# Kernel optimization log

Hardware: AMD Instinct MI355X
Metric: run time of the kernel (lower is better)

## Reference

```python
import jax, jax.numpy as jnp
import numpy as np

N = 32768      # total points (multiple of patch_size -> no padding needed)
C = 768        # channels
H = 8          # num heads
K = 256        # patch_size (window length)
HD = C // H    # head dim = 96, divisible by 6 (3 axes * rotary pairs)
FREQ = 100.0   # rope_freq


def rope3d(x, pos):
    """Point-position RoPE: head dim split into 3 axis chunks, each rotated
    by angles pos_axis * freq**(-i/half).  x: [N,H,HD], pos: [N,3] float."""
    d_axis = HD // 3            # 32
    half = d_axis // 2          # 16
    inv_freq = FREQ ** (-jnp.arange(half, dtype=x.dtype) / half)   # [half]
    ang = pos[:, :, None] * inv_freq[None, None, :]                # [N,3,half]
    cos = jnp.cos(ang)[:, None, :, :]                              # [N,1,3,half]
    sin = jnp.sin(ang)[:, None, :, :]
    xr = x.reshape(x.shape[0], x.shape[1], 3, d_axis)              # [N,H,3,d_axis]
    x1, x2 = xr[..., :half], xr[..., half:]
    out = jnp.concatenate([x1 * cos - x2 * sin, x1 * sin + x2 * cos], axis=-1)
    return out.reshape(x.shape)


def setup_inputs() -> dict:
    key = jax.random.key(0)
    ks = jax.random.split(key, 6)
    feat = jax.random.normal(ks[0], (N, C), dtype=jnp.float32)
    grid_coord = jax.random.randint(ks[1], (N, 3), 0, 1024, dtype=jnp.int32)
    order = jax.random.permutation(ks[2], N).astype(jnp.int32)     # serialized order
    inverse = jnp.argsort(order).astype(jnp.int32)                 # its inverse
    w_qkv = jax.random.normal(ks[3], (C, 3 * C), dtype=jnp.float32) * 0.02
    b_qkv = jnp.zeros((3 * C,), dtype=jnp.float32)
    w_proj = jax.random.normal(ks[4], (C, C), dtype=jnp.float32) * 0.02
    b_proj = jnp.zeros((C,), dtype=jnp.float32)
    return {"feat": feat, "grid_coord": grid_coord, "order": order,
            "inverse": inverse, "w_qkv": w_qkv, "b_qkv": b_qkv,
            "w_proj": w_proj, "b_proj": b_proj}


def reference(feat, grid_coord, order, inverse, w_qkv, b_qkv, w_proj, b_proj):
    scale = HD ** -0.5
    P = N // K  # number of windows
    qkv = (feat @ w_qkv + b_qkv)[order]                   # gather by serialized order
    pos = grid_coord[order].astype(feat.dtype)            # [N,3]
    q, k, v = jnp.split(qkv, 3, axis=-1)
    q = rope3d(q.reshape(N, H, HD), pos)
    k = rope3d(k.reshape(N, H, HD), pos)
    v = v.reshape(N, H, HD)
    # windowed (varlen with equal patch lengths) attention
    qw = q.reshape(P, K, H, HD)
    kw = k.reshape(P, K, H, HD)
    vw = v.reshape(P, K, H, HD)
    logits = jnp.einsum('pqhd,pkhd->phqk', qw, kw) * scale
    attn = jax.nn.softmax(logits, axis=-1)
    out = jnp.einsum('phqk,pkhd->pqhd', attn, vw).reshape(N, C)
    out = out[inverse]                                    # scatter back to input order
    return out @ w_proj + b_proj
```

## Files before the change

### kernel.cpp

```cpp
#include <hip/hip_runtime.h>
#include <hip/hip_bf16.h>
#include <stdint.h>

typedef __bf16 bf16_t;
typedef __bf16 bf16x8 __attribute__((ext_vector_type(8)));
typedef __bf16 bf16x4 __attribute__((ext_vector_type(4)));
typedef float f32x4 __attribute__((ext_vector_type(4)));

template <int V> struct ic { static constexpr int value = V; };

__device__ __forceinline__ void gload_lds16(const bf16_t* g, bf16_t* l) {
  __builtin_amdgcn_global_load_lds((const __attribute__((address_space(1))) void*)g,
                                   (__attribute__((address_space(3))) void*)l, 16, 0, 0);
}

__global__ __launch_bounds__(256) void transpose_cast_k(const float* __restrict__ W,
                                                        bf16_t* __restrict__ Bt,
                                                        int KDin, int MDin) {
  __shared__ float tile[64][65];
  const int bm = blockIdx.x, bk = blockIdx.y;
  const int c = threadIdx.x & 63, r0 = threadIdx.x >> 6;
#pragma unroll
  for (int rr = 0; rr < 16; ++rr) {
    int row = rr * 4 + r0;
    tile[row][c] = W[(size_t)(bk * 64 + row) * MDin + bm * 64 + c];
  }
  __syncthreads();
#pragma unroll
  for (int rr = 0; rr < 16; ++rr) {
    int mo = rr * 4 + r0;
    Bt[(size_t)(bm * 64 + mo) * KDin + bk * 64 + c] = (bf16_t)tile[c][mo];
  }
}

__global__ __launch_bounds__(256) void gather_cast_k(const float* __restrict__ feat,
                                                     const int* __restrict__ order,
                                                     const int* __restrict__ grid_coord,
                                                     bf16_t* __restrict__ featp,
                                                     float* __restrict__ posf) {
  const int id = blockIdx.x * 256 + threadIdx.x;
  const int j = id / 192;
  const int c = (id % 192) * 4;
  const int g = order[j];
  const float4 v = *(const float4*)(feat + (size_t)g * 768 + c);
  bf16x4 o;
  o[0] = (bf16_t)v.x; o[1] = (bf16_t)v.y; o[2] = (bf16_t)v.z; o[3] = (bf16_t)v.w;
  *(bf16x4*)(featp + (size_t)j * 768 + c) = o;
  if (c == 0) {
    posf[j * 3 + 0] = (float)grid_coord[g * 3 + 0];
    posf[j * 3 + 1] = (float)grid_coord[g * 3 + 1];
    posf[j * 3 + 2] = (float)grid_coord[g * 3 + 2];
  }
}

template <int MODE, int NBX>
__global__ __launch_bounds__(512, 2) void gemm256_k(const bf16_t* __restrict__ A,
                                                    const bf16_t* __restrict__ Bt,
                                                    const float* __restrict__ bias,
                                                    bf16_t* __restrict__ Cq,
                                                    bf16_t* __restrict__ Ck,
                                                    bf16_t* __restrict__ Cv,
                                                    float* __restrict__ Cf,
                                                    const int* __restrict__ order,
                                                    const float* __restrict__ posf) {
  extern __shared__ bf16_t sm[];
  bf16_t* ldsA = sm;
  bf16_t* ldsB = sm + 4 * 8192;

  const int tid = threadIdx.x;
  const int lane = tid & 63, wave = tid >> 6;
  const int wr = wave >> 2, wc = wave & 3;
  const int lq = lane & 15, lk = lane >> 4;

  const int bid = blockIdx.x;
  const int cpx = gridDim.x >> 3;
  const int rm = (bid & 7) * cpx + (bid >> 3);
  const int by = rm / NBX, bx = rm % NBX;

  const int o0 = tid, o1 = tid + 512;
  const int r0s = o0 >> 2, ls0 = (o0 & 3) ^ ((r0s >> 1) & 3);
  const int r1s = o1 >> 2, ls1 = (o1 & 3) ^ ((r1s >> 1) & 3);
  const bf16_t* pA0 = A + (size_t)(by * 256 + r0s) * 768 + ls0 * 8;
  const bf16_t* pA1 = A + (size_t)(by * 256 + r1s) * 768 + ls1 * 8;
  const bf16_t* pB0 = Bt + (size_t)(bx * 256 + r0s) * 768 + ls0 * 8;
  const bf16_t* pB1 = Bt + (size_t)(bx * 256 + r1s) * 768 + ls1 * 8;

  auto stageA = [&](int kt) {
    bf16_t* d = ldsA + ((kt & 3) << 13);
    gload_lds16(pA0 + kt * 32, d + o0 * 8);
    gload_lds16(pA1 + kt * 32, d + o1 * 8);
  };
  auto stageB = [&](int kt) {
    bf16_t* d = ldsB + ((kt & 3) << 13);
    gload_lds16(pB0 + kt * 32, d + o0 * 8);
    gload_lds16(pB1 + kt * 32, d + o1 * 8);
  };

  const int pslot = lk ^ ((lq >> 1) & 3);

  f32x4 acc[8][4] = {};

  stageA(0); stageB(0); stageA(1); stageB(1); stageA(2); stageB(2);
  asm volatile("s_waitcnt vmcnt(8)" ::: "memory");
  __builtin_amdgcn_s_barrier();
  __builtin_amdgcn_sched_barrier(0);

  auto group = [&](int t, auto VMC, auto STGC) {
    constexpr int VM = decltype(VMC)::value;
    constexpr bool STG = decltype(STGC)::value;
    const bf16_t* Ab = ldsA + ((t & 3) << 13);
    const bf16_t* Bb = ldsB + ((t & 3) << 13);
    bf16x8 af[4], bfr[4];
#pragma unroll
    for (int m = 0; m < 4; ++m)
      af[m] = *(const bf16x8*)(Ab + (wr * 128 + m * 16 + lq) * 32 + pslot * 8);
#pragma unroll
    for (int n = 0; n < 4; ++n)
      bfr[n] = *(const bf16x8*)(Bb + (wc * 64 + n * 16 + lq) * 32 + pslot * 8);
    if constexpr (STG) stageA(t + 3);
    __builtin_amdgcn_s_barrier();
    asm volatile("s_waitcnt lgkmcnt(0)" ::: "memory");
    __builtin_amdgcn_s_setprio(1);
#pragma unroll
    for (int n = 0; n < 4; ++n)
#pragma unroll
      for (int m = 0; m < 4; ++m)
        acc[m][n] = __builtin_amdgcn_mfma_f32_16x16x32_bf16(af[m], bfr[n], acc[m][n], 0, 0, 0);
    __builtin_amdgcn_s_setprio(0);
    __builtin_amdgcn_s_barrier();
#pragma unroll
    for (int m = 0; m < 4; ++m)
      af[m] = *(const bf16x8*)(Ab + (wr * 128 + 64 + m * 16 + lq) * 32 + pslot * 8);
    if constexpr (STG) stageB(t + 3);
    if constexpr (VM == 8) asm volatile("s_waitcnt vmcnt(8)" ::: "memory");
    else if constexpr (VM == 4) asm volatile("s_waitcnt vmcnt(4)" ::: "memory");
    else if constexpr (VM == 0) asm volatile("s_waitcnt vmcnt(0)" ::: "memory");
    __builtin_amdgcn_s_barrier();
    asm volatile("s_waitcnt lgkmcnt(0)" ::: "memory");
    __builtin_amdgcn_s_setprio(1);
#pragma unroll
    for (int n = 0; n < 4; ++n)
#pragma unroll
      for (int m = 0; m < 4; ++m)
        acc[4 + m][n] = __builtin_amdgcn_mfma_f32_16x16x32_bf16(af[m], bfr[n], acc[4 + m][n], 0, 0, 0);
    __builtin_amdgcn_s_setprio(0);
    __builtin_amdgcn_s_barrier();
    __builtin_amdgcn_sched_barrier(0);
  };

  for (int t = 0; t < 21; ++t) group(t, ic<8>{}, ic<1>{});
  group(21, ic<4>{}, ic<0>{});
  group(22, ic<0>{}, ic<0>{});
  group(23, ic<-1>{}, ic<0>{});

  const int colb = bx * 256 + wc * 64;
  float bcol[4];
#pragma unroll
  for (int n = 0; n < 4; ++n) bcol[n] = bias[colb + n * 16 + lq];

  if (MODE == 0) {
    const int sec = bx / 3;
    const int coll = colb - sec * 768;
    if (sec < 2) {
      bf16_t* base = sec == 0 ? Cq : Ck;
      const int a0 = (colb % 96) >> 5;
      const int a1 = ((colb + 32) % 96) >> 5;
      const float fr = exp2f(-0.41524101186f * (float)lq);
#pragma unroll
      for (int m = 0; m < 8; ++m) {
        const int rowb = by * 256 + wr * 128 + m * 16 + lk * 4;
#pragma unroll
        for (int r = 0; r < 4; ++r) {
          const int row = rowb + r;
          float s0, c0, s1, c1;
          __sincosf(posf[row * 3 + a0] * fr, &s0, &c0);
          __sincosf(posf[row * 3 + a1] * fr, &s1, &c1);
          const float x1 = acc[m][0][r] + bcol[0], x2 = acc[m][1][r] + bcol[1];
          const float y1 = acc[m][2][r] + bcol[2], y2 = acc[m][3][r] + bcol[3];
          acc[m][0][r] = x1 * c0 - x2 * s0;
          acc[m][1][r] = x1 * s0 + x2 * c0;
          acc[m][2][r] = y1 * c1 - y2 * s1;
          acc[m][3][r] = y1 * s1 + y2 * c1;
        }
#pragma unroll
        for (int n = 0; n < 4; ++n) {
          const int col = coll + n * 16 + lq;
#pragma unroll
          for (int r = 0; r < 4; ++r)
            base[(size_t)(rowb + r) * 768 + col] = (bf16_t)acc[m][n][r];
        }
      }
    } else {
#pragma unroll
      for (int m = 0; m < 8; ++m) {
        const int rowb = by * 256 + wr * 128 + m * 16 + lk * 4;
#pragma unroll
        for (int n = 0; n < 4; ++n) {
          const int col = coll + n * 16 + lq;
          bf16x4 o;
#pragma unroll
          for (int r = 0; r < 4; ++r) o[r] = (bf16_t)(acc[m][n][r] + bcol[n]);
          *(bf16x4*)(Cv + (size_t)col * 32768 + rowb) = o;
        }
      }
    }
  } else {
#pragma unroll
    for (int m = 0; m < 8; ++m) {
      const int rowb = by * 256 + wr * 128 + m * 16 + lk * 4;
      int ro[4];
#pragma unroll
      for (int r = 0; r < 4; ++r) ro[r] = order[rowb + r];
#pragma unroll
      for (int n = 0; n < 4; ++n) {
        const int col = colb + n * 16 + lq;
#pragma unroll
        for (int r = 0; r < 4; ++r)
          Cf[(size_t)ro[r] * 768 + col] = acc[m][n][r] + bcol[n];
      }
    }
  }
}

__global__ __launch_bounds__(256) void attn_k(bf16_t* QO,
                                              const bf16_t* __restrict__ Kb,
                                              const bf16_t* __restrict__ Vt) {
  __shared__ bf16_t KV[24576];
  __shared__ bf16_t Pb[4][2048];
  const int bid = blockIdx.x;
  const int chunk = bid & 3;
  const int ph = bid >> 2;
  const int h = ph & 7, p = ph >> 3;
  const int tid = threadIdx.x, lane = tid & 63, wave = tid >> 6;
  const int lq = lane & 15, lk = lane >> 4;
  const int tok0 = p * 256;
  const int qrow0 = chunk * 64 + wave * 16;
  const float scale = 0.10206207262f;

#pragma unroll
  for (int i = 0; i < 12; ++i) {
    const int fi = i * 4 + wave;
    const int nt = fi / 3, a = fi - nt * 3;
    const bf16_t* src = Kb + (size_t)(tok0 + nt * 16 + (lane & 15)) * 768 +
                        h * 96 + a * 32 + (lane >> 4) * 8;
    gload_lds16(src, KV + i * 2048 + tid * 8);
  }
  bf16x8 aq[3];
  {
    const bf16_t* qb = QO + (size_t)(tok0 + qrow0 + lq) * 768 + h * 96 + lk * 8;
#pragma unroll
    for (int kc = 0; kc < 3; ++kc) aq[kc] = *(const bf16x8*)(qb + kc * 32);
  }
  __syncthreads();

  f32x4 sacc[16];
#pragma unroll
  for (int nt = 0; nt < 16; ++nt) {
    f32x4 acc = {0.f, 0.f, 0.f, 0.f};
#pragma unroll
    for (int kc = 0; kc < 3; ++kc) {
      bf16x8 bk = *(const bf16x8*)(KV + (size_t)((nt * 3 + kc) * 64 + lane) * 8);
      acc = __builtin_amdgcn_mfma_f32_16x16x32_bf16(aq[kc], bk, acc, 0, 0, 0);
    }
    sacc[nt] = acc;
  }
  __syncthreads();

#pragma unroll
  for (int i = 0; i < 12; ++i) {
    const int fi = i * 4 + wave;
    const int d = (fi >> 3) * 16 + (lane & 15);
    const int tb = (fi & 7) * 32 + (lane >> 4) * 8;
    const bf16_t* src = Vt + (size_t)(h * 96 + d) * 32768 + tok0 + tb;
    gload_lds16(src, KV + i * 2048 + tid * 8);
  }

  float linv[4];
#pragma unroll
  for (int r = 0; r < 4; ++r) {
    float mx = -1e30f;
#pragma unroll
    for (int nt = 0; nt < 16; ++nt) mx = fmaxf(mx, sacc[nt][r]);
    mx = fmaxf(mx, __shfl_xor(mx, 1));
    mx = fmaxf(mx, __shfl_xor(mx, 2));
    mx = fmaxf(mx, __shfl_xor(mx, 4));
    mx = fmaxf(mx, __shfl_xor(mx, 8));
    mx *= scale;
    float l = 0.f;
#pragma unroll
    for (int nt = 0; nt < 16; ++nt) {
      float e = __expf(sacc[nt][r] * scale - mx);
      sacc[nt][r] = e;
      l += e;
    }
    l += __shfl_xor(l, 1);
    l += __shfl_xor(l, 2);
    l += __shfl_xor(l, 4);
    l += __shfl_xor(l, 8);
    linv[r] = 1.f / l;
  }
  __syncthreads();

  bf16_t* pw = &Pb[wave][0];
  f32x4 oacc[6] = {};
#pragma unroll
  for (int hf = 0; hf < 2; ++hf) {
#pragma unroll
    for (int ntl = 0; ntl < 8; ++ntl) {
      const int nt = hf * 8 + ntl;
      const int chk = ntl * 2 + (lq >> 3);
#pragma unroll
      for (int r = 0; r < 4; ++r) {
        const int row = lk * 4 + r;
        const int phys = chk ^ (row & 7);
        pw[row * 128 + phys * 8 + (lq & 7)] = (bf16_t)sacc[nt][r];
      }
    }
#pragma unroll
    for (int kcl = 0; kcl < 4; ++kcl) {
      const int physr = (kcl * 4 + lk) ^ (lq & 7);
      bf16x8 pf = *(const bf16x8*)(pw + lq * 128 + physr * 8);
      const int kc = hf * 4 + kcl;
#pragma unroll
      for (int dt = 0; dt < 6; ++dt) {
        bf16x8 vb = *(const bf16x8*)(KV + (size_t)((dt * 8 + kc) * 64 + lane) * 8);
        oacc[dt] = __builtin_amdgcn_mfma_f32_16x16x32_bf16(pf, vb, oacc[dt], 0, 0, 0);
      }
    }
  }

#pragma unroll
  for (int dt = 0; dt < 6; ++dt) {
#pragma unroll
    for (int r = 0; r < 4; ++r) {
      const int row = tok0 + qrow0 + lk * 4 + r;
      QO[(size_t)row * 768 + h * 96 + dt * 16 + lq] = (bf16_t)(oacc[dt][r] * linv[r]);
    }
  }
}

extern "C" void kernel_launch(void* const* d_in, const int* in_sizes, int n_in,
                              void* d_out, int out_size, void* d_ws, size_t ws_size,
                              hipStream_t stream) {
  const float* feat       = (const float*)d_in[0];
  const int*   grid_coord = (const int*)d_in[1];
  const int*   order      = (const int*)d_in[2];
  const float* w_qkv      = (const float*)d_in[4];
  const float* b_qkv      = (const float*)d_in[5];
  const float* w_proj     = (const float*)d_in[6];
  const float* b_proj     = (const float*)d_in[7];
  float* out = (float*)d_out;

  char* ws = (char*)d_ws;
  bf16_t* Bt1   = (bf16_t*)(ws);
  bf16_t* Bt2   = (bf16_t*)(ws + 3538944);
  bf16_t* featp = (bf16_t*)(ws + 4718592);
  bf16_t* Qb    = (bf16_t*)(ws + 55050240);
  bf16_t* Kb    = (bf16_t*)(ws + 105381888);
  bf16_t* Vt    = (bf16_t*)(ws + 155713536);
  float*  posf  = (float*)(ws + 206045184);

  static bool attr_set = false;
  if (!attr_set) {
    (void)hipFuncSetAttribute((const void*)gemm256_k<0, 9>,
                              hipFuncAttributeMaxDynamicSharedMemorySize, 131072);
    (void)hipFuncSetAttribute((const void*)gemm256_k<1, 3>,
                              hipFuncAttributeMaxDynamicSharedMemorySize, 131072);
    attr_set = true;
  }

  transpose_cast_k<<<dim3(36, 12), 256, 0, stream>>>(w_qkv, Bt1, 768, 2304);
  transpose_cast_k<<<dim3(12, 12), 256, 0, stream>>>(w_proj, Bt2, 768, 768);
  gather_cast_k<<<24576, 256, 0, stream>>>(feat, order, grid_coord, featp, posf);
  gemm256_k<0, 9><<<1152, 512, 131072, stream>>>(featp, Bt1, b_qkv, Qb, Kb, Vt,
                                                 nullptr, nullptr, posf);
  attn_k<<<4096, 256, 0, stream>>>(Qb, Kb, Vt);
  gemm256_k<1, 3><<<384, 512, 131072, stream>>>(Qb, Bt2, b_proj, nullptr, nullptr,
                                                nullptr, out, order, nullptr);
}
```

Baseline: 483.7 us.

## Process full window per attention block and overlap V load with QK

The attention kernel now assigns one (window, head) pair per 512-thread block. Each of the 8 waves handles two 16-row query tiles, replacing four 256-thread blocks that each reloaded the same K and V tiles. K and V are loaded into separate regions of a 128KB dynamic LDS buffer up front. Split vmcnt waits let the V transfer overlap the first QK^T and softmax pass. This removes redundant global traffic for K/V, but the large LDS footprint limits residency to one block per CU, and each wave's two row tiles run serially.

Measured after the change: 484.3 us. About the same (+0.1%).

```diff
diff --git a/kernel.cpp b/kernel.cpp
--- a/kernel.cpp
+++ b/kernel.cpp
@@ -222,119 +222,127 @@
   }
 }
 
-__global__ __launch_bounds__(256) void attn_k(bf16_t* QO,
+__global__ __launch_bounds__(512) void attn_k(bf16_t* QO,
                                               const bf16_t* __restrict__ Kb,
                                               const bf16_t* __restrict__ Vt) {
-  __shared__ bf16_t KV[24576];
-  __shared__ bf16_t Pb[4][2048];
+  extern __shared__ bf16_t alds[];
+  bf16_t* Kreg = alds;
+  bf16_t* Vreg = alds + 24576;
   const int bid = blockIdx.x;
-  const int chunk = bid & 3;
-  const int ph = bid >> 2;
-  const int h = ph & 7, p = ph >> 3;
+  const int h = bid & 7, p = bid >> 3;
   const int tid = threadIdx.x, lane = tid & 63, wave = tid >> 6;
   const int lq = lane & 15, lk = lane >> 4;
   const int tok0 = p * 256;
-  const int qrow0 = chunk * 64 + wave * 16;
   const float scale = 0.10206207262f;
-
-#pragma unroll
-  for (int i = 0; i < 12; ++i) {
-    const int fi = i * 4 + wave;
+  bf16_t* pw = alds + 49152 + wave * 2048;
+
+  bf16x8 aq[2][3];
+#pragma unroll
+  for (int rb = 0; rb < 2; ++rb) {
+    const bf16_t* qb = QO + (size_t)(tok0 + wave * 32 + rb * 16 + lq) * 768 + h * 96 + lk * 8;
+#pragma unroll
+    for (int kc = 0; kc < 3; ++kc) aq[rb][kc] = *(const bf16x8*)(qb + kc * 32);
+  }
+  __builtin_amdgcn_sched_barrier(0);
+
+#pragma unroll
+  for (int i = 0; i < 6; ++i) {
+    const int fi = i * 8 + wave;
     const int nt = fi / 3, a = fi - nt * 3;
     const bf16_t* src = Kb + (size_t)(tok0 + nt * 16 + (lane & 15)) * 768 +
                         h * 96 + a * 32 + (lane >> 4) * 8;
-    gload_lds16(src, KV + i * 2048 + tid * 8);
-  }
-  bf16x8 aq[3];
-  {
-    const bf16_t* qb = QO + (size_t)(tok0 + qrow0 + lq) * 768 + h * 96 + lk * 8;
-#pragma unroll
-    for (int kc = 0; kc < 3; ++kc) aq[kc] = *(const bf16x8*)(qb + kc * 32);
-  }
-  __syncthreads();
-
-  f32x4 sacc[16];
-#pragma unroll
-  for (int nt = 0; nt < 16; ++nt) {
-    f32x4 acc = {0.f, 0.f, 0.f, 0.f};
-#pragma unroll
-    for (int kc = 0; kc < 3; ++kc) {
-      bf16x8 bk = *(const bf16x8*)(KV + (size_t)((nt * 3 + kc) * 64 + lane) * 8);
-      acc = __builtin_amdgcn_mfma_f32_16x16x32_bf16(aq[kc], bk, acc, 0, 0, 0);
-    }
-    sacc[nt] = acc;
-  }
-  __syncthreads();
-
-#pragma unroll
-  for (int i = 0; i < 12; ++i) {
-    const int fi = i * 4 + wave;
+    gload_lds16(src, Kreg + i * 4096 + tid * 8);
+  }
+#pragma unroll
+  for (int i = 0; i < 6; ++i) {
+    const int fi = i * 8 + wave;
     const int d = (fi >> 3) * 16 + (lane & 15);
     const int tb = (fi & 7) * 32 + (lane >> 4) * 8;
     const bf16_t* src = Vt + (size_t)(h * 96 + d) * 32768 + tok0 + tb;
-    gload_lds16(src, KV + i * 2048 + tid * 8);
-  }
-
-  float linv[4];
-#pragma unroll
-  for (int r = 0; r < 4; ++r) {
-    float mx = -1e30f;
-#pragma unroll
-    for (int nt = 0; nt < 16; ++nt) mx = fmaxf(mx, sacc[nt][r]);
-    mx = fmaxf(mx, __shfl_xor(mx, 1));
-    mx = fmaxf(mx, __shfl_xor(mx, 2));
-    mx = fmaxf(mx, __shfl_xor(mx, 4));
-    mx = fmaxf(mx, __shfl_xor(mx, 8));
-    mx *= scale;
-    float l = 0.f;
+    gload_lds16(src, Vreg + i * 4096 + tid * 8);
+  }
+
+  asm volatile("s_waitcnt vmcnt(6)" ::: "memory");
+  __builtin_amdgcn_s_barrier();
+
+#pragma unroll
+  for (int rb = 0; rb < 2; ++rb) {
+    f32x4 sacc[16];
 #pragma unroll
     for (int nt = 0; nt < 16; ++nt) {
-      float e = __expf(sacc[nt][r] * scale - mx);
-      sacc[nt][r] = e;
-      l += e;
-    }
-    l += __shfl_xor(l, 1);
-    l += __shfl_xor(l, 2);
-    l += __shfl_xor(l, 4);
-    l += __shfl_xor(l, 8);
-    linv[r] = 1.f / l;
-  }
-  __syncthreads();
-
-  bf16_t* pw = &Pb[wave][0];
-  f32x4 oacc[6] = {};
-#pragma unroll
-  for (int hf = 0; hf < 2; ++hf) {
-#pragma unroll
-    for (int ntl = 0; ntl < 8; ++ntl) {
-      const int nt = hf * 8 + ntl;
-      const int chk = ntl * 2 + (lq >> 3);
+      f32x4 acc = {0.f, 0.f, 0.f, 0.f};
+#pragma unroll
+      for (int kc = 0; kc < 3; ++kc) {
+        bf16x8 bk = *(const bf16x8*)(Kreg + (size_t)((nt * 3 + kc) * 64 + lane) * 8);
+        acc = __builtin_amdgcn_mfma_f32_16x16x32_bf16(aq[rb][kc], bk, acc, 0, 0, 0);
+      }
+      sacc[nt] = acc;
+    }
+
+    float linv[4];
+#pragma unroll
+    for (int r = 0; r < 4; ++r) {
+      float mx = -1e30f;
+#pragma unroll
+      for (int nt = 0; nt < 16; ++nt) mx = fmaxf(mx, sacc[nt][r]);
+      mx = fmaxf(mx, __shfl_xor(mx, 1));
+      mx = fmaxf(mx, __shfl_xor(mx, 2));
+      mx = fmaxf(mx, __shfl_xor(mx, 4));
+      mx = fmaxf(mx, __shfl_xor(mx, 8));
+      mx *= scale;
+      float l = 0.f;
+#pragma unroll
+      for (int nt = 0; nt < 16; ++nt) {
+        float e = __expf(sacc[nt][r] * scale - mx);
+        sacc[nt][r] = e;
+        l += e;
+      }
+      l += __shfl_xor(l, 1);
+      l += __shfl_xor(l, 2);
+      l += __shfl_xor(l, 4);
+      l += __shfl_xor(l, 8);
+      linv[r] = 1.f / l;
+    }
+
+    if (rb == 0) {
+      asm volatile("s_waitcnt vmcnt(0)" ::: "memory");
+      __builtin_amdgcn_s_barrier();
+    }
+
+    f32x4 oacc[6] = {};
+#pragma unroll
+    for (int hf = 0; hf < 2; ++hf) {
+#pragma unroll
+      for (int ntl = 0; ntl < 8; ++ntl) {
+        const int nt = hf * 8 + ntl;
+        const int chk = ntl * 2 + (lq >> 3);
+#pragma unroll
+        for (int r = 0; r < 4; ++r) {
+          const int row = lk * 4 + r;
+          const int phys = chk ^ (row & 7);
+          pw[row * 128 + phys * 8 + (lq & 7)] = (bf16_t)sacc[nt][r];
+        }
+      }
+#pragma unroll
+      for (int kcl = 0; kcl < 4; ++kcl) {
+        const int physr = (kcl * 4 + lk) ^ (lq & 7);
+        bf16x8 pf = *(const bf16x8*)(pw + lq * 128 + physr * 8);
+        const int kc = hf * 4 + kcl;
+#pragma unroll
+        for (int dt = 0; dt < 6; ++dt) {
+          bf16x8 vb = *(const bf16x8*)(Vreg + (size_t)((dt * 8 + kc) * 64 + lane) * 8);
+          oacc[dt] = __builtin_amdgcn_mfma_f32_16x16x32_bf16(pf, vb, oacc[dt], 0, 0, 0);
+        }
+      }
+    }
+
+#pragma unroll
+    for (int dt = 0; dt < 6; ++dt) {
 #pragma unroll
       for (int r = 0; r < 4; ++r) {
-        const int row = lk * 4 + r;
-        const int phys = chk ^ (row & 7);
-        pw[row * 128 + phys * 8 + (lq & 7)] = (bf16_t)sacc[nt][r];
-      }
-    }
-#pragma unroll
-    for (int kcl = 0; kcl < 4; ++kcl) {
-      const int physr = (kcl * 4 + lk) ^ (lq & 7);
-      bf16x8 pf = *(const bf16x8*)(pw + lq * 128 + physr * 8);
-      const int kc = hf * 4 + kcl;
-#pragma unroll
-      for (int dt = 0; dt < 6; ++dt) {
-        bf16x8 vb = *(const bf16x8*)(KV + (size_t)((dt * 8 + kc) * 64 + lane) * 8);
-        oacc[dt] = __builtin_amdgcn_mfma_f32_16x16x32_bf16(pf, vb, oacc[dt], 0, 0, 0);
-      }
-    }
-  }
-
-#pragma unroll
-  for (int dt = 0; dt < 6; ++dt) {
-#pragma unroll
-    for (int r = 0; r < 4; ++r) {
-      const int row = tok0 + qrow0 + lk * 4 + r;
-      QO[(size_t)row * 768 + h * 96 + dt * 16 + lq] = (bf16_t)(oacc[dt][r] * linv[r]);
+        const int row = tok0 + wave * 32 + rb * 16 + lk * 4 + r;
+        QO[(size_t)row * 768 + h * 96 + dt * 16 + lq] = (bf16_t)(oacc[dt][r] * linv[r]);
+      }
     }
   }
 }
@@ -366,6 +374,8 @@
                               hipFuncAttributeMaxDynamicSharedMemorySize, 131072);
     (void)hipFuncSetAttribute((const void*)gemm256_k<1, 3>,
                               hipFuncAttributeMaxDynamicSharedMemorySize, 131072);
+    (void)hipFuncSetAttribute((const void*)attn_k,
+                              hipFuncAttributeMaxDynamicSharedMemorySize, 131072);
     attr_set = true;
   }
 
@@ -374,7 +384,7 @@
   gather_cast_k<<<24576, 256, 0, stream>>>(feat, order, grid_coord, featp, posf);
   gemm256_k<0, 9><<<1152, 512, 131072, stream>>>(featp, Bt1, b_qkv, Qb, Kb, Vt,
                                                  nullptr, nullptr, posf);
-  attn_k<<<4096, 256, 0, stream>>>(Qb, Kb, Vt);
+  attn_k<<<1024, 512, 131072, stream>>>(Qb, Kb, Vt);
   gemm256_k<1, 3><<<384, 512, 131072, stream>>>(Qb, Bt2, b_proj, nullptr, nullptr,
                                                 nullptr, out, order, nullptr);
 }
```
